# Optimization experiments

Measured on AMD Instinct MI355X. Metric: run time of the kernel, lower is better.

Reference implementation:

```python
import jax, jax.numpy as jnp
import numpy as np

B, N_NODES, T_IN = 512, 32, 12
HID, HEADS, OUT_CH, DEG = 64, 8, 9, 8


def setup_inputs() -> dict:
    key = jax.random.key(0)
    ks = jax.random.split(key, 26)
    rn = lambda k, s, sc=0.1: (jax.random.normal(k, s, jnp.float32) * sc)
    E = B * N_NODES * DEG
    src = jax.random.randint(ks[0], (E,), 0, N_NODES, jnp.int32)
    dst = jax.random.randint(ks[1], (E,), 0, N_NODES, jnp.int32)
    off = jnp.repeat(jnp.arange(B, dtype=jnp.int32) * N_NODES, N_NODES * DEG)
    edge_index = jnp.stack([src + off, dst + off])  # block-diagonal batched graph
    x = jax.random.normal(ks[2], (B, N_NODES, T_IN), jnp.float32)
    return {
        "x": x,
        "edge_index": edge_index,
        # gat1: in=T_IN -> HEADS*HID, concat
        "W1": rn(ks[3], (T_IN, HEADS * HID)),
        "a_src1": rn(ks[4], (HEADS, HID)),
        "a_dst1": rn(ks[5], (HEADS, HID)),
        "b1": rn(ks[6], (HEADS * HID,), 0.01),
        # gat2: in=HEADS*HID -> HID, heads=1, mean (concat=False)
        "W2": rn(ks[7], (HEADS * HID, HID), 0.05),
        "a_src2": rn(ks[8], (1, HID)),
        "a_dst2": rn(ks[9], (1, HID)),
        "b2": rn(ks[10], (HID,), 0.01),
        "gamma": jnp.ones((HID,), jnp.float32),
        "beta": jnp.zeros((HID,), jnp.float32),
        # gru1: input_size=N_NODES(=32), hidden=HID
        "Wi1": rn(ks[11], (3 * HID, N_NODES)),
        "Wh1": rn(ks[12], (3 * HID, HID)),
        "bi1": rn(ks[13], (3 * HID,), 0.01),
        "bh1": rn(ks[14], (3 * HID,), 0.01),
        # gru2: input_size=HID, hidden=HID
        "Wi2": rn(ks[15], (3 * HID, HID)),
        "Wh2": rn(ks[16], (3 * HID, HID)),
        "bi2": rn(ks[17], (3 * HID,), 0.01),
        "bh2": rn(ks[18], (3 * HID,), 0.01),
        "Wf": rn(ks[19], (OUT_CH, HID)),
        "bf": rn(ks[20], (OUT_CH,), 0.01),
    }


def _gat_layer(x, src, dst, W, a_s, a_d, b, concat):
    # PyG GATConv (eval mode, self-loops already appended by caller)
    Nn = x.shape[0]
    heads, hc = a_s.shape
    h = (x @ W).reshape(Nn, heads, hc)                 # [N, H, C]
    es = jnp.sum(h * a_s, axis=-1)                     # [N, H]
    ed = jnp.sum(h * a_d, axis=-1)
    e = jax.nn.leaky_relu(es[src] + ed[dst], 0.2)      # [E, H]
    m = jax.ops.segment_max(e, dst, num_segments=Nn)
    p = jnp.exp(e - m[dst])
    s = jax.ops.segment_sum(p, dst, num_segments=Nn)
    alpha = p / (s[dst] + 1e-16)                       # per-dst softmax
    out = jax.ops.segment_sum(h[src] * alpha[:, :, None], dst, num_segments=Nn)
    out = out.reshape(Nn, heads * hc) if concat else out.mean(axis=1)
    return out + b


def _gru(x, Wi, Wh, bi, bh):
    # torch.nn.GRU (batch_first) single layer; x: [B, T, F]
    H = Wh.shape[1]
    xi = x @ Wi.T + bi                                 # [B, T, 3H]
    def step(h, xt):
        gh = h @ Wh.T + bh
        r = jax.nn.sigmoid(xt[:, :H] + gh[:, :H])
        z = jax.nn.sigmoid(xt[:, H:2 * H] + gh[:, H:2 * H])
        n = jnp.tanh(xt[:, 2 * H:] + r * gh[:, 2 * H:])
        hn = (1.0 - z) * n + z * h
        return hn, hn
    h0 = jnp.zeros((x.shape[0], H), x.dtype)
    _, ys = jax.lax.scan(step, h0, jnp.swapaxes(xi, 0, 1))
    return jnp.swapaxes(ys, 0, 1)


def reference(x, edge_index, W1, a_src1, a_dst1, b1, W2, a_src2, a_dst2, b2,
              gamma, beta, Wi1, Wh1, bi1, bh1, Wi2, Wh2, bi2, bh2, Wf, bf):
    Bsz, Nn_, T = x.shape
    Nn = Bsz * Nn_
    xf = x.reshape(Nn, T)                              # dropout is identity in eval
    sl = jnp.arange(Nn, dtype=edge_index.dtype)        # PyG add_self_loops=True
    src = jnp.concatenate([edge_index[0], sl])
    dst = jnp.concatenate([edge_index[1], sl])
    h = jax.nn.elu(_gat_layer(xf, src, dst, W1, a_src1, a_dst1, b1, True))
    h = jax.nn.elu(_gat_layer(h, src, dst, W2, a_src2, a_dst2, b2, False))
    mu = h.mean(-1, keepdims=True)
    var = ((h - mu) ** 2).mean(-1, keepdims=True)
    h = (h - mu) / jnp.sqrt(var + 1e-5) * gamma + beta
    seq = h.reshape(Bsz, Nn_, -1).transpose(0, 2, 1)   # [B, HID(seq), N_NODES(feat)]
    g = _gru(seq, Wi1, Wh1, bi1, bh1)
    g = _gru(g, Wi2, Wh2, bi2, bh2)
    return g[:, -1, :] @ Wf.T + bf                     # [B, OUT_CH]
```

## Files before the change

kernel.cpp:

```cpp
#include <hip/hip_runtime.h>
#include <hip/hip_bf16.h>
#include <stdint.h>

#define BATCH 512
#define NN 32
#define T_IN 12
#define HID 64
#define HEADS 8
#define OUT_CH 9
#define EPB (NN*8)
#define ETOT (EPB+NN)
#define F1 (HEADS*HID)

using u16 = unsigned short;
using u32 = unsigned int;
typedef _Float16 f16;
typedef _Float16 f16x2 __attribute__((ext_vector_type(2)));
typedef u32 v4u __attribute__((ext_vector_type(4)));

__device__ __forceinline__ float bf2f(u16 u){ return __uint_as_float(((u32)u)<<16); }
__device__ __forceinline__ u16 f2bf(float f){
    u32 x = __float_as_uint(f);
    u32 r = (x + 0x7FFFu + ((x>>16)&1u))>>16;
    return (u16)r;
}
__device__ __forceinline__ u32 packf16(float a, float b){
    f16x2 p; p.x=(f16)a; p.y=(f16)b; return __builtin_bit_cast(u32,p);
}
__device__ __forceinline__ u16 f2h16(float a){ f16 h=(f16)a; return __builtin_bit_cast(u16,h); }
__device__ __forceinline__ float lof(u32 w){ return (float)__builtin_bit_cast(f16x2,w).x; }
__device__ __forceinline__ float hif(u32 w){ return (float)__builtin_bit_cast(f16x2,w).y; }
__device__ __forceinline__ float dot2(u32 a, u32 b, float c){
#if __has_builtin(__builtin_amdgcn_fdot2)
    return __builtin_amdgcn_fdot2(__builtin_bit_cast(f16x2,a), __builtin_bit_cast(f16x2,b), c, false);
#else
    return fmaf(lof(a),lof(b), fmaf(hif(a),hif(b), c));
#endif
}
__device__ __forceinline__ float elu1(float x){ return x > 0.f ? x : (__expf(x)-1.f); }
__device__ __forceinline__ float sigm(float x){ return 1.f/(1.f+__expf(-x)); }
__device__ __forceinline__ float tanh_(float x){ return 1.f - 2.f/(__expf(2.f*x)+1.f); }
__device__ __forceinline__ u32 fenc(float v){
    u32 b=__float_as_uint(v);
    return (b&0x80000000u) ? ~b : (b|0x80000000u);
}
__device__ __forceinline__ float fdec(u32 k){
    return __uint_as_float((k&0x80000000u) ? (k&0x7FFFFFFFu) : ~k);
}

#define DOT4(acc,A,W) do{ acc=dot2(A.x,W.x,acc); acc=dot2(A.y,W.y,acc); \
                          acc=dot2(A.z,W.z,acc); acc=dot2(A.w,W.w,acc); }while(0)
#define DOT8(acc,A0,A1,W0,W1) do{ DOT4(acc,A0,W0); DOT4(acc,A1,W1); }while(0)

__global__ __launch_bounds__(256) void k_detect(const u32* __restrict__ xw, int* __restrict__ flag){
    __shared__ int cnt;
    if(threadIdx.x==0) cnt=0;
    __syncthreads();
    int c=0;
    for(int i=threadIdx.x;i<4096;i+=256){
        u32 w=xw[i];
        if(w & 0x7FFFFFFFu){
            u32 el=(w>>7)&0xFFu;
            if(el>=0x90u) c++;
        }
    }
    atomicAdd(&cnt,c);
    __syncthreads();
    if(threadIdx.x==0) *flag = (cnt>256) ? 1 : 0;
}

struct CvtDesc {
    const void* src[16];
    void*       dst[16];
    int         n[16];
};

__global__ __launch_bounds__(256) void k_convert(CvtDesc d, const int* __restrict__ flag){
    const int seg = blockIdx.x;
    const int f = *flag;
    const void* s = d.src[seg];
    const int n = d.n[seg];
    const int stride = gridDim.y*256;
    float* o=(float*)d.dst[seg];
    for(int i=blockIdx.y*256+threadIdx.x;i<n;i+=stride)
        o[i] = f ? ((const float*)s)[i] : bf2f(((const u16*)s)[i]);
}

__global__ __launch_bounds__(256) void k_w2i(const void* __restrict__ W2src, u16* __restrict__ W2i,
                                             const int* __restrict__ flag){
    int i = blockIdx.x*256+threadIdx.x;
    int k=i>>6, j=i&63;
    float v = (*flag)? ((const float*)W2src)[i] : bf2f(((const u16*)W2src)[i]);
    W2i[ (((size_t)(k>>3)*64 + j)<<3) + (k&7) ] = f2h16(v);
}

__global__ __launch_bounds__(256) void k_wpk(
    const void* __restrict__ Wi1, const void* __restrict__ Wh1,
    const void* __restrict__ Wi2, const void* __restrict__ Wh2,
    u32* __restrict__ wpk, const int* __restrict__ flag)
{
    int w = blockIdx.x*256+threadIdx.x;
    int m = w/6144;
    int rem = w - m*6144;
    int row = rem>>5, kw = rem&31;
    const void* s = (m==0)?Wi1 : (m==1)?Wh1 : (m==2)?Wi2 : Wh2;
    int K = (m==0)?32:64;
    int f=*flag;
    int k0=2*kw, k1=k0+1;
    float v0=0.f, v1=0.f;
    if(k0<K) v0 = f? ((const float*)s)[row*K+k0] : bf2f(((const u16*)s)[row*K+k0]);
    if(k1<K) v1 = f? ((const float*)s)[row*K+k1] : bf2f(((const u16*)s)[row*K+k1]);
    wpk[w]=packf16(v0,v1);
}

__global__ __launch_bounds__(256,2) void k_gat1(
    const float* __restrict__ x, const int* __restrict__ ei,
    const float* __restrict__ W1, const float* __restrict__ a_s, const float* __restrict__ a_d,
    const float* __restrict__ b1, u32* __restrict__ h1g)
{
    const int b = blockIdx.x, t = threadIdx.x;
    __shared__ __align__(16) float s_x[NN][12];
    __shared__ float s_W1[T_IN*F1];
    __shared__ __align__(16) u16 s_h[NN][520];
    __shared__ __align__(16) u32 s_aspk[HEADS*32], s_adpk[HEADS*32];
    __shared__ float s_es[NN][HEADS], s_ed[NN][HEADS];
    __shared__ unsigned char s_src[ETOT], s_dst[ETOT];
    __shared__ float s_al[ETOT][HEADS];
    __shared__ u32 s_mx[NN*HEADS];
    __shared__ float s_sm[NN*HEADS], s_inv[NN*HEADS];
    __shared__ int s_cnt[NN], s_off[NN], s_fil[NN];
    __shared__ short s_lst[ETOT];

    for(int i=t;i<NN*T_IN;i+=256) s_x[i/12][i%12] = x[b*NN*T_IN + i];
    for(int i=t;i<T_IN*F1;i+=256) s_W1[i]=W1[i];
    s_aspk[t]=packf16(a_s[2*t],a_s[2*t+1]);
    s_adpk[t]=packf16(a_d[2*t],a_d[2*t+1]);
    s_mx[t]=0u; s_sm[t]=0.f;
    if(t<EPB){
        s_src[t] = (unsigned char)(ei[b*EPB+t] - b*NN);
        s_dst[t] = (unsigned char)(ei[(size_t)BATCH*EPB + b*EPB+t] - b*NN);
    }
    if(t<NN){ s_src[EPB+t]=s_dst[EPB+t]=(unsigned char)t; s_cnt[t]=0; s_fil[t]=0; }
    __syncthreads();

    {
        float w0[12], w1[12];
        #pragma unroll
        for(int k=0;k<12;k++){ w0[k]=s_W1[k*F1+t]; w1[k]=s_W1[k*F1+t+256]; }
        for(int n=0;n<NN;n++){
            const float4* xp=(const float4*)s_x[n];
            float4 xa=xp[0], xb=xp[1], xc=xp[2];
            float A=0.f,B=0.f;
            A=fmaf(xa.x,w0[0],A); A=fmaf(xa.y,w0[1],A); A=fmaf(xa.z,w0[2],A); A=fmaf(xa.w,w0[3],A);
            A=fmaf(xb.x,w0[4],A); A=fmaf(xb.y,w0[5],A); A=fmaf(xb.z,w0[6],A); A=fmaf(xb.w,w0[7],A);
            A=fmaf(xc.x,w0[8],A); A=fmaf(xc.y,w0[9],A); A=fmaf(xc.z,w0[10],A); A=fmaf(xc.w,w0[11],A);
            B=fmaf(xa.x,w1[0],B); B=fmaf(xa.y,w1[1],B); B=fmaf(xa.z,w1[2],B); B=fmaf(xa.w,w1[3],B);
            B=fmaf(xb.x,w1[4],B); B=fmaf(xb.y,w1[5],B); B=fmaf(xb.z,w1[6],B); B=fmaf(xb.w,w1[7],B);
            B=fmaf(xc.x,w1[8],B); B=fmaf(xc.y,w1[9],B); B=fmaf(xc.z,w1[10],B); B=fmaf(xc.w,w1[11],B);
            s_h[n][t]=f2h16(A); s_h[n][t+256]=f2h16(B);
        }
    }
    for(int e=t;e<ETOT;e+=256) atomicAdd(&s_cnt[s_dst[e]],1);
    __syncthreads();

    {
        int n=t&31, hd=t>>5;
        const v4u* hp=(const v4u*)((const u16*)s_h[n] + hd*64);
        v4u h0=hp[0],h1=hp[1],h2=hp[2],h3=hp[3],h4=hp[4],h5=hp[5],h6=hp[6],h7=hp[7];
        const v4u* ap=(const v4u*)&s_aspk[hd*32];
        const v4u* dp=(const v4u*)&s_adpk[hd*32];
        float e1=0.f,e2=0.f;
        { v4u w=ap[0]; DOT4(e1,h0,w); w=ap[1]; DOT4(e1,h1,w); w=ap[2]; DOT4(e1,h2,w); w=ap[3]; DOT4(e1,h3,w);
          w=ap[4]; DOT4(e1,h4,w); w=ap[5]; DOT4(e1,h5,w); w=ap[6]; DOT4(e1,h6,w); w=ap[7]; DOT4(e1,h7,w); }
        { v4u w=dp[0]; DOT4(e2,h0,w); w=dp[1]; DOT4(e2,h1,w); w=dp[2]; DOT4(e2,h2,w); w=dp[3]; DOT4(e2,h3,w);
          w=dp[4]; DOT4(e2,h4,w); w=dp[5]; DOT4(e2,h5,w); w=dp[6]; DOT4(e2,h6,w); w=dp[7]; DOT4(e2,h7,w); }
        s_es[n][hd]=e1; s_ed[n][hd]=e2;
    }
    if(t==0){ int o=0; for(int i=0;i<NN;i++){ s_off[i]=o; o+=s_cnt[i]; } }
    __syncthreads();

    for(int e=t;e<ETOT;e+=256){
        int d=s_dst[e]; int p=atomicAdd(&s_fil[d],1); s_lst[s_off[d]+p]=(short)e;
    }
    for(int i=t;i<ETOT*HEADS;i+=256){
        int e=i>>3, hd=i&7;
        int sr=s_src[e], d=s_dst[e];
        float v = s_es[sr][hd]+s_ed[d][hd];
        v = v>0.f? v : 0.2f*v;
        s_al[e][hd]=v;
        atomicMax(&s_mx[d*8+hd], fenc(v));
    }
    __syncthreads();

    for(int i=t;i<ETOT*HEADS;i+=256){
        int e=i>>3, hd=i&7;
        int d=s_dst[e];
        float p=__expf(s_al[e][hd]-fdec(s_mx[d*8+hd]));
        s_al[e][hd]=p;
        atomicAdd(&s_sm[d*8+hd], p);
    }
    __syncthreads();
    s_inv[t]=1.f/(s_sm[t]+1e-16f);
    __syncthreads();

    {
        int d=t&31, hd=t>>5;
        int o=s_off[d], cnt=s_cnt[d];
        float inv=s_inv[d*8+hd];
        size_t obase = ((size_t)(b*NN+d))*256 + hd*32;
        #pragma unroll
        for(int ch=0;ch<2;ch++){
            float acc[32];
            #pragma unroll
            for(int i=0;i<32;i++) acc[i]=0.f;
            for(int i=0;i<cnt;i++){
                int e=s_lst[o+i]; float a=s_al[e][hd]; int sr=s_src[e];
                const v4u* hp=(const v4u*)((const u16*)s_h[sr] + hd*64 + ch*32);
                v4u p0=hp[0],p1=hp[1],p2=hp[2],p3=hp[3];
                #define ACC2(i,w) acc[2*(i)]+=a*lof(w); acc[2*(i)+1]+=a*hif(w);
                ACC2(0,p0.x) ACC2(1,p0.y) ACC2(2,p0.z) ACC2(3,p0.w)
                ACC2(4,p1.x) ACC2(5,p1.y) ACC2(6,p1.z) ACC2(7,p1.w)
                ACC2(8,p2.x) ACC2(9,p2.y) ACC2(10,p2.z) ACC2(11,p2.w)
                ACC2(12,p3.x) ACC2(13,p3.y) ACC2(14,p3.z) ACC2(15,p3.w)
                #undef ACC2
            }
            u32* op = h1g + obase + ch*16;
            #pragma unroll
            for(int j=0;j<16;j++){
                float v0=elu1(acc[2*j]*inv   + b1[hd*64+ch*32+2*j]);
                float v1=elu1(acc[2*j+1]*inv + b1[hd*64+ch*32+2*j+1]);
                op[j]=packf16(v0,v1);
            }
        }
    }
}

__global__ __launch_bounds__(256,2) void k_gat2ln(
    const u32* __restrict__ h1g, const int* __restrict__ ei,
    const uint4* __restrict__ W2i, const float* __restrict__ a_s2, const float* __restrict__ a_d2,
    const float* __restrict__ b2, const float* __restrict__ gam, const float* __restrict__ bet,
    float* __restrict__ hlng)
{
    const int b=blockIdx.x, t=threadIdx.x;
    __shared__ __align__(16) u32 s_h1[NN*260];
    __shared__ float s_h2[NN][HID];
    __shared__ float s_es[NN], s_ed[NN];
    __shared__ unsigned char s_src[ETOT], s_dst[ETOT];
    __shared__ float s_al[ETOT];
    __shared__ u32 s_mx[NN];
    __shared__ float s_sm[NN], s_inv[NN];
    __shared__ int s_cnt[NN], s_off[NN], s_fil[NN];
    __shared__ short s_lst[ETOT];

    { const u32* g = h1g + (size_t)b*8192;
      for(int w=t; w<8192; w+=256){ int n=w>>8, c=w&255; s_h1[n*260+c]=g[w]; } }
    if(t<EPB){
        s_src[t]=(unsigned char)(ei[b*EPB+t]-b*NN);
        s_dst[t]=(unsigned char)(ei[(size_t)BATCH*EPB+b*EPB+t]-b*NN);
    }
    if(t<NN){ s_src[EPB+t]=s_dst[EPB+t]=(unsigned char)t;
              s_cnt[t]=0; s_fil[t]=0; s_mx[t]=0u; s_sm[t]=0.f; }
    __syncthreads();

    for(int e=t;e<ETOT;e+=256) atomicAdd(&s_cnt[s_dst[e]],1);
    {
        int n0=(t>>5)<<2, j0=(t&31)<<1;
        const u32* r0=&s_h1[(n0+0)*260];
        const u32* r1=&s_h1[(n0+1)*260];
        const u32* r2=&s_h1[(n0+2)*260];
        const u32* r3=&s_h1[(n0+3)*260];
        float a00=0,a01=0,a10=0,a11=0,a20=0,a21=0,a30=0,a31=0;
        for(int kb=0;kb<64;kb++){
            uint4 A0=*(const uint4*)&r0[kb*4];
            uint4 A1=*(const uint4*)&r1[kb*4];
            uint4 A2=*(const uint4*)&r2[kb*4];
            uint4 A3=*(const uint4*)&r3[kb*4];
            const uint4* wp=&W2i[kb*64+j0];
            uint4 w0=wp[0], w1=wp[1];
            a00=dot2(A0.x,w0.x,a00); a00=dot2(A0.y,w0.y,a00); a00=dot2(A0.z,w0.z,a00); a00=dot2(A0.w,w0.w,a00);
            a01=dot2(A0.x,w1.x,a01); a01=dot2(A0.y,w1.y,a01); a01=dot2(A0.z,w1.z,a01); a01=dot2(A0.w,w1.w,a01);
            a10=dot2(A1.x,w0.x,a10); a10=dot2(A1.y,w0.y,a10); a10=dot2(A1.z,w0.z,a10); a10=dot2(A1.w,w0.w,a10);
            a11=dot2(A1.x,w1.x,a11); a11=dot2(A1.y,w1.y,a11); a11=dot2(A1.z,w1.z,a11); a11=dot2(A1.w,w1.w,a11);
            a20=dot2(A2.x,w0.x,a20); a20=dot2(A2.y,w0.y,a20); a20=dot2(A2.z,w0.z,a20); a20=dot2(A2.w,w0.w,a20);
            a21=dot2(A2.x,w1.x,a21); a21=dot2(A2.y,w1.y,a21); a21=dot2(A2.z,w1.z,a21); a21=dot2(A2.w,w1.w,a21);
            a30=dot2(A3.x,w0.x,a30); a30=dot2(A3.y,w0.y,a30); a30=dot2(A3.z,w0.z,a30); a30=dot2(A3.w,w0.w,a30);
            a31=dot2(A3.x,w1.x,a31); a31=dot2(A3.y,w1.y,a31); a31=dot2(A3.z,w1.z,a31); a31=dot2(A3.w,w1.w,a31);
        }
        s_h2[n0+0][j0]=a00; s_h2[n0+0][j0+1]=a01;
        s_h2[n0+1][j0]=a10; s_h2[n0+1][j0+1]=a11;
        s_h2[n0+2][j0]=a20; s_h2[n0+2][j0+1]=a21;
        s_h2[n0+3][j0]=a30; s_h2[n0+3][j0+1]=a31;
    }
    __syncthreads();

    {
        int n=t>>3, g=t&7;
        float e1=0,e2=0;
        #pragma unroll
        for(int cc=0; cc<8; cc++){
            float hv = s_h2[n][g*8+cc];
            e1 += hv*a_s2[g*8+cc];
            e2 += hv*a_d2[g*8+cc];
        }
        #pragma unroll
        for(int m=1;m<8;m<<=1){ e1 += __shfl_xor(e1,m,64); e2 += __shfl_xor(e2,m,64); }
        if(g==0){ s_es[n]=e1; s_ed[n]=e2; }
    }
    if(t==0){ int o=0; for(int i=0;i<NN;i++){ s_off[i]=o; o+=s_cnt[i]; } }
    __syncthreads();

    for(int e=t;e<ETOT;e+=256){
        int d=s_dst[e]; int p=atomicAdd(&s_fil[d],1); s_lst[s_off[d]+p]=(short)e;
    }
    for(int e=t;e<ETOT;e+=256){
        int d=s_dst[e];
        float v = s_es[s_src[e]] + s_ed[d];
        v = v>0.f? v:0.2f*v;
        s_al[e]=v;
        atomicMax(&s_mx[d], fenc(v));
    }
    __syncthreads();

    for(int e=t;e<ETOT;e+=256){
        int d=s_dst[e];
        float p=__expf(s_al[e]-fdec(s_mx[d]));
        s_al[e]=p;
        atomicAdd(&s_sm[d], p);
    }
    __syncthreads();
    if(t<NN) s_inv[t]=1.f/(s_sm[t]+1e-16f);
    __syncthreads();

    {
        int n=t>>3, g=t&7;
        float acc[8];
        #pragma unroll
        for(int i=0;i<8;i++) acc[i]=0;
        int o=s_off[n], cnt=s_cnt[n];
        float inv=s_inv[n];
        for(int i=0;i<cnt;i++){
            int e=s_lst[o+i]; float a=s_al[e]; int sr=s_src[e];
            const float4* hp=(const float4*)&s_h2[sr][g*8];
            float4 v0=hp[0], v1=hp[1];
            acc[0]+=a*v0.x; acc[1]+=a*v0.y; acc[2]+=a*v0.z; acc[3]+=a*v0.w;
            acc[4]+=a*v1.x; acc[5]+=a*v1.y; acc[6]+=a*v1.z; acc[7]+=a*v1.w;
        }
        float sum=0,sq=0;
        #pragma unroll
        for(int i=0;i<8;i++){
            float v = elu1(acc[i]*inv + b2[g*8+i]);
            acc[i]=v; sum+=v; sq+=v*v;
        }
        #pragma unroll
        for(int m=1;m<8;m<<=1){ sum+=__shfl_xor(sum,m,64); sq+=__shfl_xor(sq,m,64); }
        float mu = sum*(1.f/64.f);
        float var = sq*(1.f/64.f) - mu*mu;
        float rs = rsqrtf(var + 1e-5f);
        float* outp = hlng + (size_t)b*HID*NN;
        #pragma unroll
        for(int i=0;i<8;i++){
            int c=g*8+i;
            float v=(acc[i]-mu)*rs*gam[c] + bet[c];
            outp[c*NN + n] = v;
        }
    }
}

__global__ __launch_bounds__(512,1) void k_gruf(
    const float* __restrict__ hlng, const u32* __restrict__ wpk,
    const float* __restrict__ bi1, const float* __restrict__ bh1,
    const float* __restrict__ bi2, const float* __restrict__ bh2,
    const float* __restrict__ Wf, const float* __restrict__ bfv,
    void* __restrict__ outp, const int* __restrict__ flag)
{
    const int b=blockIdx.x, t=threadIdx.x;
    const int wave=t>>6, lane=t&63;
    const int layer=wave>>2;
    const int uu=lane&15, kq=lane>>4;
    const int u=(wave&3)*16+uu;

    __shared__ __align__(16) u32 s_x1[64][32];
    __shared__ __align__(16) u32 s_h1[2][32];
    __shared__ __align__(16) u32 s_h2[2][32];
    __shared__ float s_h2f[64];

    {   const float2* g=(const float2*)(hlng + (size_t)b*2048);
        for(int w=t;w<2048;w+=512){
            int step=w>>5, j=w&31;
            u32 v=0u;
            if(j<16){ float2 f=g[step*16+j]; v=packf16(f.x,f.y); }
            s_x1[step][j]=v;
        }
    }
    if(t<32){ s_h1[0][t]=0u; s_h1[1][t]=0u; s_h2[0][t]=0u; s_h2[1][t]=0u; }

    const v4u* wi4 = (const v4u*)(wpk + (size_t)(layer*2+0)*6144);
    const v4u* wh4 = (const v4u*)(wpk + (size_t)(layer*2+1)*6144);
    const int q2 = kq*2;
    v4u wiR0=wi4[(u     )*8+q2], wiR1=wi4[(u     )*8+q2+1];
    v4u wiZ0=wi4[(64+u  )*8+q2], wiZ1=wi4[(64+u  )*8+q2+1];
    v4u wiN0=wi4[(128+u )*8+q2], wiN1=wi4[(128+u )*8+q2+1];
    v4u whR0=wh4[(u     )*8+q2], whR1=wh4[(u     )*8+q2+1];
    v4u whZ0=wh4[(64+u  )*8+q2], whZ1=wh4[(64+u  )*8+q2+1];
    v4u whN0=wh4[(128+u )*8+q2], whN1=wh4[(128+u )*8+q2+1];

    const float* bi = layer? bi2:bi1;
    const float* bh = layer? bh2:bh1;
    float br=bi[u]+bh[u], bz=bi[64+u]+bh[64+u], bxn=bi[128+u], bhn=bh[128+u];

    asm volatile("" : "+v"(wiR0),"+v"(wiR1),"+v"(wiZ0),"+v"(wiZ1),"+v"(wiN0),"+v"(wiN1),
                      "+v"(whR0),"+v"(whR1),"+v"(whZ0),"+v"(whZ1),"+v"(whN0),"+v"(whN1),
                      "+v"(br),"+v"(bz),"+v"(bxn),"+v"(bhn));

    float h=0.f;
    __syncthreads();

    for(int it=0; it<=64; ++it){
        const int pb=(it-1)&1, cb=it&1;
        const bool act = layer ? (it>=1) : (it<64);
        const int xi = (it<64)? it : 0;
        const v4u* xp = layer ? (const v4u*)&s_h1[pb][kq*8] : (const v4u*)&s_x1[xi][kq*8];
        const v4u* hp = layer ? (const v4u*)&s_h2[pb][kq*8] : (const v4u*)&s_h1[pb][kq*8];
        v4u xa=xp[0], xb=xp[1];
        v4u ha=hp[0], hb=hp[1];
        float pr=0.f,pz=0.f,pxn=0.f,phn=0.f;
        DOT8(pr , xa,xb, wiR0,wiR1);
        DOT8(pz , xa,xb, wiZ0,wiZ1);
        DOT8(pxn, xa,xb, wiN0,wiN1);
        DOT8(pr , ha,hb, whR0,whR1);
        DOT8(pz , ha,hb, whZ0,whZ1);
        DOT8(phn, ha,hb, whN0,whN1);
        pr +=__shfl_xor(pr ,16,64); pz +=__shfl_xor(pz ,16,64);
        pxn+=__shfl_xor(pxn,16,64); phn+=__shfl_xor(phn,16,64);
        pr +=__shfl_xor(pr ,32,64); pz +=__shfl_xor(pz ,32,64);
        pxn+=__shfl_xor(pxn,32,64); phn+=__shfl_xor(phn,32,64);
        float r=sigm(pr+br), z=sigm(pz+bz);
        float n=tanh_(pxn+bxn + r*(phn+bhn));
        float hn=(1.f-z)*n + z*h;
        h = act ? hn : h;
        if(act && kq==0){
            u16 hv=f2h16(h);
            if(layer==0) ((u16*)s_h1[cb])[u]=hv;
            else { ((u16*)s_h2[cb])[u]=hv; if(it==64) s_h2f[u]=h; }
        }
        __syncthreads();
    }

    if(t<OUT_CH){
        float acc=bfv[t];
        const float4* wp=(const float4*)(Wf + t*64);
        const float4* hp=(const float4*)s_h2f;
        #pragma unroll
        for(int k=0;k<16;k++){
            float4 w=wp[k], v=hp[k];
            acc += w.x*v.x + w.y*v.y + w.z*v.z + w.w*v.w;
        }
        if(*flag) ((float*)outp)[b*OUT_CH+t]=acc;
        else      ((u16*)outp)[b*OUT_CH+t]=f2bf(acc);
    }
}

extern "C" void kernel_launch(void* const* d_in, const int* in_sizes, int n_in,
                              void* d_out, int out_size, void* d_ws, size_t ws_size,
                              hipStream_t stream)
{
    char* ws=(char*)d_ws;
    int* flag = (int*)ws;
    float* cf = (float*)(ws + 256);
    float* c_x   = cf; cf+=196608;
    float* c_W1  = cf; cf+=6144;
    float* c_as1 = cf; cf+=512;
    float* c_ad1 = cf; cf+=512;
    float* c_b1  = cf; cf+=512;
    float* c_as2 = cf; cf+=64;
    float* c_ad2 = cf; cf+=64;
    float* c_b2  = cf; cf+=64;
    float* c_gam = cf; cf+=64;
    float* c_bet = cf; cf+=64;
    float* c_bi1 = cf; cf+=192;
    float* c_bh1 = cf; cf+=192;
    float* c_bi2 = cf; cf+=192;
    float* c_bh2 = cf; cf+=192;
    float* c_Wf  = cf; cf+=576;
    float* c_bf  = cf; cf+=9;
    uintptr_t p = ((uintptr_t)cf + 255) & ~(uintptr_t)255;
    u16* c_W2i = (u16*)p;
    p = (p + 32768*2 + 255) & ~(uintptr_t)255;
    u32* wpk = (u32*)p;
    p = (p + 24576*4 + 255) & ~(uintptr_t)255;
    u32* h1g = (u32*)p;
    p = (p + (size_t)BATCH*NN*256*4 + 255) & ~(uintptr_t)255;
    float* hlng = (float*)p;

    const int* ei = (const int*)d_in[1];

    CvtDesc d;
    const int srcIdx[16] = {0,2,3,4,5,7,8,9,10,11,14,15,18,19,20,21};
    void* dsts[16] = {c_x,c_W1,c_as1,c_ad1,c_b1,c_as2,c_ad2,c_b2,c_gam,c_bet,
                      c_bi1,c_bh1,c_bi2,c_bh2,c_Wf,c_bf};
    const int ns[16] = {196608,6144,512,512,512,64,64,64,64,64,
                        192,192,192,192,576,9};
    for(int i=0;i<16;i++){ d.src[i]=d_in[srcIdx[i]]; d.dst[i]=dsts[i]; d.n[i]=ns[i]; }

    k_detect <<<dim3(1),dim3(256),0,stream>>>((const u32*)d_in[0], flag);
    k_convert<<<dim3(16,8),dim3(256),0,stream>>>(d, flag);
    k_w2i    <<<dim3(128),dim3(256),0,stream>>>(d_in[6], c_W2i, flag);
    k_wpk    <<<dim3(96),dim3(256),0,stream>>>(d_in[12],d_in[13],d_in[16],d_in[17], wpk, flag);
    k_gat1   <<<dim3(BATCH),dim3(256),0,stream>>>(c_x,ei,c_W1,c_as1,c_ad1,c_b1,h1g);
    k_gat2ln <<<dim3(BATCH),dim3(256),0,stream>>>(h1g,ei,(const uint4*)c_W2i,c_as2,c_ad2,c_b2,c_gam,c_bet,hlng);
    k_gruf   <<<dim3(BATCH),dim3(512),0,stream>>>(hlng,wpk,c_bi1,c_bh1,c_bi2,c_bh2,c_Wf,c_bf,d_out,flag);
}
```

Baseline: 253.9 us.

## Split fused GRU into input-projection kernels and single-wave recurrent kernels

Replaces the single fused two-layer GRU kernel with four kernels. Two kernels precompute the input projections (Wi·x + bi) for all 64 timesteps in parallel and store them as fp16. Two single-wavefront kernels then run only the hidden-state recurrence per layer, with no block barriers or cross-lane shuffle reductions. The cost is that the two layers no longer overlap and each recurrent step becomes a long serial chain of dot products per thread. It also adds extra launches and global round-trips for the projections and the layer-1 outputs, and leaves low occupancy of one wave per block.

```diff
diff --git a/kernel.cpp b/kernel.cpp
--- a/kernel.cpp
+++ b/kernel.cpp
@@ -28,6 +28,7 @@
     f16x2 p; p.x=(f16)a; p.y=(f16)b; return __builtin_bit_cast(u32,p);
 }
 __device__ __forceinline__ u16 f2h16(float a){ f16 h=(f16)a; return __builtin_bit_cast(u16,h); }
+__device__ __forceinline__ float h16f(u16 v){ f16 h=__builtin_bit_cast(f16,v); return (float)h; }
 __device__ __forceinline__ float lof(u32 w){ return (float)__builtin_bit_cast(f16x2,w).x; }
 __device__ __forceinline__ float hif(u32 w){ return (float)__builtin_bit_cast(f16x2,w).y; }
 __device__ __forceinline__ float dot2(u32 a, u32 b, float c){
@@ -50,7 +51,9 @@
 
 #define DOT4(acc,A,W) do{ acc=dot2(A.x,W.x,acc); acc=dot2(A.y,W.y,acc); \
                           acc=dot2(A.z,W.z,acc); acc=dot2(A.w,W.w,acc); }while(0)
-#define DOT8(acc,A0,A1,W0,W1) do{ DOT4(acc,A0,W0); DOT4(acc,A1,W1); }while(0)
+#define DOT32(acc,A0,A1,A2,A3,A4,A5,A6,A7,W0,W1,W2,W3,W4,W5,W6,W7) do{ \
+    DOT4(acc,A0,W0); DOT4(acc,A1,W1); DOT4(acc,A2,W2); DOT4(acc,A3,W3); \
+    DOT4(acc,A4,W4); DOT4(acc,A5,W5); DOT4(acc,A6,W6); DOT4(acc,A7,W7); }while(0)
 
 __global__ __launch_bounds__(256) void k_detect(const u32* __restrict__ xw, int* __restrict__ flag){
     __shared__ int cnt;
@@ -366,97 +369,145 @@
     }
 }
 
-__global__ __launch_bounds__(512,1) void k_gruf(
+__global__ __launch_bounds__(256,2) void k_xi1(
     const float* __restrict__ hlng, const u32* __restrict__ wpk,
-    const float* __restrict__ bi1, const float* __restrict__ bh1,
-    const float* __restrict__ bi2, const float* __restrict__ bh2,
-    const float* __restrict__ Wf, const float* __restrict__ bfv,
+    const float* __restrict__ bi1, u16* __restrict__ xi1)
+{
+    const int b=blockIdx.x, t=threadIdx.x;
+    __shared__ __align__(16) u32 s_x[64*16];
+    { const float2* g=(const float2*)(hlng + (size_t)b*2048);
+      for(int w=t;w<1024;w+=256){ float2 f=g[w]; s_x[w]=packf16(f.x,f.y); } }
+    __syncthreads();
+    if(t<192){
+        const v4u* wr=(const v4u*)(wpk) + t*8;
+        v4u w0=wr[0],w1=wr[1],w2=wr[2],w3=wr[3];
+        float bias=bi1[t];
+        u16* o = xi1 + (size_t)b*12288 + t;
+        for(int step=0;step<64;step++){
+            const v4u* xp=(const v4u*)&s_x[step*16];
+            v4u xa=xp[0],xb=xp[1],xc=xp[2],xd=xp[3];
+            float a=bias;
+            DOT4(a,xa,w0); DOT4(a,xb,w1); DOT4(a,xc,w2); DOT4(a,xd,w3);
+            o[step*192]=f2h16(a);
+        }
+    }
+}
+
+__global__ __launch_bounds__(256,2) void k_xi2(
+    const u16* __restrict__ y1, const u32* __restrict__ wpk,
+    const float* __restrict__ bi2, u16* __restrict__ xi2)
+{
+    const int b=blockIdx.x, t=threadIdx.x;
+    __shared__ __align__(16) u32 s_y[64*32];
+    { const v4u* g=(const v4u*)(y1 + (size_t)b*4096);
+      v4u* s=(v4u*)s_y;
+      for(int w=t;w<512;w+=256) s[w]=g[w]; }
+    __syncthreads();
+    if(t<192){
+        const v4u* wr=(const v4u*)(wpk + 2*6144) + t*8;
+        v4u w0=wr[0],w1=wr[1],w2=wr[2],w3=wr[3],w4=wr[4],w5=wr[5],w6=wr[6],w7=wr[7];
+        float bias=bi2[t];
+        u16* o = xi2 + (size_t)b*12288 + t;
+        for(int step=0;step<64;step++){
+            const v4u* xp=(const v4u*)&s_y[step*32];
+            v4u a0=xp[0],a1=xp[1],a2=xp[2],a3=xp[3],a4=xp[4],a5=xp[5],a6=xp[6],a7=xp[7];
+            float a=bias;
+            DOT32(a,a0,a1,a2,a3,a4,a5,a6,a7,w0,w1,w2,w3,w4,w5,w6,w7);
+            o[step*192]=f2h16(a);
+        }
+    }
+}
+
+__global__ __launch_bounds__(64,1) void k_gru1s(
+    const u32* __restrict__ xi1, const u32* __restrict__ wpk,
+    const float* __restrict__ bh1, u16* __restrict__ y1)
+{
+    const int b=blockIdx.x, u=threadIdx.x;
+    __shared__ __align__(16) u32 s_xi[64*96];
+    __shared__ __align__(16) u32 s_h[32];
+    { const v4u* g=(const v4u*)(xi1 + (size_t)b*6144);
+      v4u* s=(v4u*)s_xi;
+      for(int w=u;w<1536;w+=64) s[w]=g[w]; }
+    const v4u* wh=(const v4u*)(wpk + 6144);
+    v4u r0=wh[u*8+0],r1=wh[u*8+1],r2=wh[u*8+2],r3=wh[u*8+3],
+        r4=wh[u*8+4],r5=wh[u*8+5],r6=wh[u*8+6],r7=wh[u*8+7];
+    v4u z0=wh[(64+u)*8+0],z1=wh[(64+u)*8+1],z2=wh[(64+u)*8+2],z3=wh[(64+u)*8+3],
+        z4=wh[(64+u)*8+4],z5=wh[(64+u)*8+5],z6=wh[(64+u)*8+6],z7=wh[(64+u)*8+7];
+    v4u n0=wh[(128+u)*8+0],n1=wh[(128+u)*8+1],n2=wh[(128+u)*8+2],n3=wh[(128+u)*8+3],
+        n4=wh[(128+u)*8+4],n5=wh[(128+u)*8+5],n6=wh[(128+u)*8+6],n7=wh[(128+u)*8+7];
+    float bhr=bh1[u], bhz=bh1[64+u], bhn=bh1[128+u];
+    if(u<32) s_h[u]=0u;
+    __syncthreads();
+    u16* yo = y1 + (size_t)b*4096;
+    float h=0.f;
+    for(int t=0;t<64;t++){
+        const u16* xr=(const u16*)(s_xi) + t*192;
+        float xir=h16f(xr[u]), xiz=h16f(xr[64+u]), xin=h16f(xr[128+u]);
+        const v4u* hp=(const v4u*)s_h;
+        v4u A0=hp[0],A1=hp[1],A2=hp[2],A3=hp[3],A4=hp[4],A5=hp[5],A6=hp[6],A7=hp[7];
+        float gr=bhr,gz=bhz,gn=bhn;
+        DOT32(gr,A0,A1,A2,A3,A4,A5,A6,A7,r0,r1,r2,r3,r4,r5,r6,r7);
+        DOT32(gz,A0,A1,A2,A3,A4,A5,A6,A7,z0,z1,z2,z3,z4,z5,z6,z7);
+        DOT32(gn,A0,A1,A2,A3,A4,A5,A6,A7,n0,n1,n2,n3,n4,n5,n6,n7);
+        float rr=sigm(xir+gr), zz=sigm(xiz+gz);
+        float nn=tanh_(xin + rr*gn);
+        h=(1.f-zz)*nn+zz*h;
+        u16 hv=f2h16(h);
+        ((u16*)s_h)[u]=hv;
+        yo[t*64+u]=hv;
+    }
+}
+
+__global__ __launch_bounds__(64,1) void k_gru2s(
+    const u32* __restrict__ xi2, const u32* __restrict__ wpk,
+    const float* __restrict__ bh2, const float* __restrict__ Wf, const float* __restrict__ bfv,
     void* __restrict__ outp, const int* __restrict__ flag)
 {
-    const int b=blockIdx.x, t=threadIdx.x;
-    const int wave=t>>6, lane=t&63;
-    const int layer=wave>>2;
-    const int uu=lane&15, kq=lane>>4;
-    const int u=(wave&3)*16+uu;
-
-    __shared__ __align__(16) u32 s_x1[64][32];
-    __shared__ __align__(16) u32 s_h1[2][32];
-    __shared__ __align__(16) u32 s_h2[2][32];
-    __shared__ float s_h2f[64];
-
-    {   const float2* g=(const float2*)(hlng + (size_t)b*2048);
-        for(int w=t;w<2048;w+=512){
-            int step=w>>5, j=w&31;
-            u32 v=0u;
-            if(j<16){ float2 f=g[step*16+j]; v=packf16(f.x,f.y); }
-            s_x1[step][j]=v;
-        }
-    }
-    if(t<32){ s_h1[0][t]=0u; s_h1[1][t]=0u; s_h2[0][t]=0u; s_h2[1][t]=0u; }
-
-    const v4u* wi4 = (const v4u*)(wpk + (size_t)(layer*2+0)*6144);
-    const v4u* wh4 = (const v4u*)(wpk + (size_t)(layer*2+1)*6144);
-    const int q2 = kq*2;
-    v4u wiR0=wi4[(u     )*8+q2], wiR1=wi4[(u     )*8+q2+1];
-    v4u wiZ0=wi4[(64+u  )*8+q2], wiZ1=wi4[(64+u  )*8+q2+1];
-    v4u wiN0=wi4[(128+u )*8+q2], wiN1=wi4[(128+u )*8+q2+1];
-    v4u whR0=wh4[(u     )*8+q2], whR1=wh4[(u     )*8+q2+1];
-    v4u whZ0=wh4[(64+u  )*8+q2], whZ1=wh4[(64+u  )*8+q2+1];
-    v4u whN0=wh4[(128+u )*8+q2], whN1=wh4[(128+u )*8+q2+1];
-
-    const float* bi = layer? bi2:bi1;
-    const float* bh = layer? bh2:bh1;
-    float br=bi[u]+bh[u], bz=bi[64+u]+bh[64+u], bxn=bi[128+u], bhn=bh[128+u];
-
-    asm volatile("" : "+v"(wiR0),"+v"(wiR1),"+v"(wiZ0),"+v"(wiZ1),"+v"(wiN0),"+v"(wiN1),
-                      "+v"(whR0),"+v"(whR1),"+v"(whZ0),"+v"(whZ1),"+v"(whN0),"+v"(whN1),
-                      "+v"(br),"+v"(bz),"+v"(bxn),"+v"(bhn));
-
+    const int b=blockIdx.x, u=threadIdx.x;
+    __shared__ __align__(16) u32 s_xi[64*96];
+    __shared__ __align__(16) u32 s_h[32];
+    __shared__ float s_hf[64];
+    { const v4u* g=(const v4u*)(xi2 + (size_t)b*6144);
+      v4u* s=(v4u*)s_xi;
+      for(int w=u;w<1536;w+=64) s[w]=g[w]; }
+    const v4u* wh=(const v4u*)(wpk + 3*6144);
+    v4u r0=wh[u*8+0],r1=wh[u*8+1],r2=wh[u*8+2],r3=wh[u*8+3],
+        r4=wh[u*8+4],r5=wh[u*8+5],r6=wh[u*8+6],r7=wh[u*8+7];
+    v4u z0=wh[(64+u)*8+0],z1=wh[(64+u)*8+1],z2=wh[(64+u)*8+2],z3=wh[(64+u)*8+3],
+        z4=wh[(64+u)*8+4],z5=wh[(64+u)*8+5],z6=wh[(64+u)*8+6],z7=wh[(64+u)*8+7];
+    v4u n0=wh[(128+u)*8+0],n1=wh[(128+u)*8+1],n2=wh[(128+u)*8+2],n3=wh[(128+u)*8+3],
+        n4=wh[(128+u)*8+4],n5=wh[(128+u)*8+5],n6=wh[(128+u)*8+6],n7=wh[(128+u)*8+7];
+    float bhr=bh2[u], bhz=bh2[64+u], bhn=bh2[128+u];
+    if(u<32) s_h[u]=0u;
+    __syncthreads();
     float h=0.f;
-    __syncthreads();
-
-    for(int it=0; it<=64; ++it){
-        const int pb=(it-1)&1, cb=it&1;
-        const bool act = layer ? (it>=1) : (it<64);
-        const int xi = (it<64)? it : 0;
-        const v4u* xp = layer ? (const v4u*)&s_h1[pb][kq*8] : (const v4u*)&s_x1[xi][kq*8];
-        const v4u* hp = layer ? (const v4u*)&s_h2[pb][kq*8] : (const v4u*)&s_h1[pb][kq*8];
-        v4u xa=xp[0], xb=xp[1];
-        v4u ha=hp[0], hb=hp[1];
-        float pr=0.f,pz=0.f,pxn=0.f,phn=0.f;
-        DOT8(pr , xa,xb, wiR0,wiR1);
-        DOT8(pz , xa,xb, wiZ0,wiZ1);
-        DOT8(pxn, xa,xb, wiN0,wiN1);
-        DOT8(pr , ha,hb, whR0,whR1);
-        DOT8(pz , ha,hb, whZ0,whZ1);
-        DOT8(phn, ha,hb, whN0,whN1);
-        pr +=__shfl_xor(pr ,16,64); pz +=__shfl_xor(pz ,16,64);
-        pxn+=__shfl_xor(pxn,16,64); phn+=__shfl_xor(phn,16,64);
-        pr +=__shfl_xor(pr ,32,64); pz +=__shfl_xor(pz ,32,64);
-        pxn+=__shfl_xor(pxn,32,64); phn+=__shfl_xor(phn,32,64);
-        float r=sigm(pr+br), z=sigm(pz+bz);
-        float n=tanh_(pxn+bxn + r*(phn+bhn));
-        float hn=(1.f-z)*n + z*h;
-        h = act ? hn : h;
-        if(act && kq==0){
-            u16 hv=f2h16(h);
-            if(layer==0) ((u16*)s_h1[cb])[u]=hv;
-            else { ((u16*)s_h2[cb])[u]=hv; if(it==64) s_h2f[u]=h; }
-        }
-        __syncthreads();
-    }
-
-    if(t<OUT_CH){
-        float acc=bfv[t];
-        const float4* wp=(const float4*)(Wf + t*64);
-        const float4* hp=(const float4*)s_h2f;
+    for(int t=0;t<64;t++){
+        const u16* xr=(const u16*)(s_xi) + t*192;
+        float xir=h16f(xr[u]), xiz=h16f(xr[64+u]), xin=h16f(xr[128+u]);
+        const v4u* hp=(const v4u*)s_h;
+        v4u A0=hp[0],A1=hp[1],A2=hp[2],A3=hp[3],A4=hp[4],A5=hp[5],A6=hp[6],A7=hp[7];
+        float gr=bhr,gz=bhz,gn=bhn;
+        DOT32(gr,A0,A1,A2,A3,A4,A5,A6,A7,r0,r1,r2,r3,r4,r5,r6,r7);
+        DOT32(gz,A0,A1,A2,A3,A4,A5,A6,A7,z0,z1,z2,z3,z4,z5,z6,z7);
+        DOT32(gn,A0,A1,A2,A3,A4,A5,A6,A7,n0,n1,n2,n3,n4,n5,n6,n7);
+        float rr=sigm(xir+gr), zz=sigm(xiz+gz);
+        float nn=tanh_(xin + rr*gn);
+        h=(1.f-zz)*nn+zz*h;
+        ((u16*)s_h)[u]=f2h16(h);
+    }
+    s_hf[u]=h;
+    __syncthreads();
+    if(u<OUT_CH){
+        float acc=bfv[u];
+        const float4* wp=(const float4*)(Wf + u*64);
+        const float4* hp=(const float4*)s_hf;
         #pragma unroll
         for(int k=0;k<16;k++){
             float4 w=wp[k], v=hp[k];
             acc += w.x*v.x + w.y*v.y + w.z*v.z + w.w*v.w;
         }
-        if(*flag) ((float*)outp)[b*OUT_CH+t]=acc;
-        else      ((u16*)outp)[b*OUT_CH+t]=f2bf(acc);
+        if(*flag) ((float*)outp)[b*OUT_CH+u]=acc;
+        else      ((u16*)outp)[b*OUT_CH+u]=f2bf(acc);
     }
 }
 
@@ -491,6 +542,9 @@
     u32* h1g = (u32*)p;
     p = (p + (size_t)BATCH*NN*256*4 + 255) & ~(uintptr_t)255;
     float* hlng = (float*)p;
+    p = (p + (size_t)BATCH*HID*NN*4 + 255) & ~(uintptr_t)255;
+    u16* y1 = (u16*)p;
+    u32* xi = h1g;
 
     const int* ei = (const int*)d_in[1];
 
@@ -508,5 +562,8 @@
     k_wpk    <<<dim3(96),dim3(256),0,stream>>>(d_in[12],d_in[13],d_in[16],d_in[17], wpk, flag);
     k_gat1   <<<dim3(BATCH),dim3(256),0,stream>>>(c_x,ei,c_W1,c_as1,c_ad1,c_b1,h1g);
     k_gat2ln <<<dim3(BATCH),dim3(256),0,stream>>>(h1g,ei,(const uint4*)c_W2i,c_as2,c_ad2,c_b2,c_gam,c_bet,hlng);
-    k_gruf   <<<dim3(BATCH),dim3(512),0,stream>>>(hlng,wpk,c_bi1,c_bh1,c_bi2,c_bh2,c_Wf,c_bf,d_out,flag);
-}
+    k_xi1    <<<dim3(BATCH),dim3(256),0,stream>>>(hlng, wpk, c_bi1, (u16*)xi);
+    k_gru1s  <<<dim3(BATCH),dim3(64),0,stream>>>(xi, wpk, c_bh1, y1);
+    k_xi2    <<<dim3(BATCH),dim3(256),0,stream>>>(y1, wpk, c_bi2, (u16*)xi);
+    k_gru2s  <<<dim3(BATCH),dim3(64),0,stream>>>(xi, wpk, c_bh2, c_Wf, c_bf, d_out, flag);
+}
```

New measurement: 282.2 us. 11.1% more time.
